# Kernel tuning notes

Measured on AMD Instinct MI355X. Metric: run time of the kernel, lower is better.

The kernel has to match this reference:

```python
import jax, jax.numpy as jnp
import numpy as np

N, E, H, ED, S = 20000, 320000, 256, 64, 4  # nodes, edges, hidden, edge_dim, message_steps


def setup_inputs() -> dict:
    key = jax.random.key(0)
    ks = jax.random.split(key, 20)
    w = lambda k, shape: jax.random.normal(k, shape, dtype=jnp.float32) * 0.02
    inp = {
        "node_state": jax.random.normal(ks[0], (N, H), dtype=jnp.float32),
        "edge_attr": jax.random.normal(ks[1], (E, ED), dtype=jnp.float32),
        # per-step stacked parameters (S steps)
        "nn_g": jnp.ones((S, H), jnp.float32),  # node_norm gamma
        "nn_b": jnp.zeros((S, H), jnp.float32),
        "mn_g": jnp.ones((S, H), jnp.float32),  # msg_norm gamma
        "mn_b": jnp.zeros((S, H), jnp.float32),
        "eW1": w(ks[2], (S, 2 * H + ED, H)), "eb1": jnp.zeros((S, H), jnp.float32),
        "eW2": w(ks[3], (S, H, H)),          "eb2": jnp.zeros((S, H), jnp.float32),
        "nW1": w(ks[4], (S, 2 * H, 2 * H)),  "nb1": jnp.zeros((S, 2 * H), jnp.float32),
        "nW2": w(ks[5], (S, 2 * H, H)),      "nb2": jnp.zeros((S, H), jnp.float32),
        "edge_index": jax.random.randint(ks[6], (2, E), 0, N, dtype=jnp.int64),
    }
    return inp


def _layer_norm(x, g, b, eps=1e-5):
    m = jnp.mean(x, axis=-1, keepdims=True)
    v = jnp.var(x, axis=-1, keepdims=True)
    return (x - m) * jax.lax.rsqrt(v + eps) * g + b


def reference(node_state, edge_attr, nn_g, nn_b, mn_g, mn_b,
              eW1, eb1, eW2, eb2, nW1, nb1, nW2, nb2, edge_index):
    n = node_state.shape[0]
    src, dst = edge_index[0], edge_index[1]
    ones = jnp.ones((dst.shape[0], 1), node_state.dtype)
    deg = jax.ops.segment_sum(ones, dst, num_segments=n)  # [N,1], same each step
    deg = jnp.maximum(deg, 1.0)
    h = node_state
    for i in range(nn_g.shape[0]):  # fixed small number of message steps
        hn = _layer_norm(h, nn_g[i], nn_b[i])                       # [N,H]
        x = jnp.concatenate([hn[src], hn[dst], edge_attr], axis=1)  # [E,2H+ED]
        msg = jax.nn.silu(x @ eW1[i] + eb1[i]) @ eW2[i] + eb2[i]    # [E,H]
        agg = jax.ops.segment_sum(msg, dst, num_segments=n)         # [N,H]
        agg = _layer_norm(agg / deg, mn_g[i], mn_b[i])
        y = jnp.concatenate([hn, agg], axis=1)                      # [N,2H]
        h = h + (jax.nn.silu(y @ nW1[i] + nb1[i]) @ nW2[i] + nb2[i])
    return h
```

## Files before the change

### kernel.cpp

```cpp
#include <hip/hip_runtime.h>
#include <hip/hip_bf16.h>
#include <stdint.h>

#define NN 20000
#define NE 320000
#define HH 256
#define EDK 64
#define NSTEPS 4
#define ECH 160000
#define NCHUNK 2
#define WSTEP 606208

typedef __attribute__((ext_vector_type(8))) short bf16x8;
typedef __attribute__((ext_vector_type(4))) float f32x4;

__device__ __forceinline__ float silu_f(float x) { return x / (1.0f + __expf(-x)); }

__device__ __forceinline__ unsigned short f2bf(float f) {
    __hip_bfloat16 h = __float2bfloat16(f);
    return __builtin_bit_cast(unsigned short, h);
}
__device__ __forceinline__ float bf2f(unsigned short u) {
    unsigned int x = ((unsigned int)u) << 16;
    return __builtin_bit_cast(float, x);
}
__device__ __forceinline__ unsigned int pk2(float a, float b) {
    return (unsigned int)f2bf(a) | ((unsigned int)f2bf(b) << 16);
}

__global__ void ln_kernel(const float* __restrict__ x, const float* __restrict__ g,
                          const float* __restrict__ b, unsigned short* __restrict__ y, int M)
{
    int row  = blockIdx.x * 4 + (threadIdx.x >> 6);
    int lane = threadIdx.x & 63;
    if (row >= M) return;
    float4 v = *(const float4*)(x + (size_t)row * HH + lane * 4);
    float s  = v.x + v.y + v.z + v.w;
    float ss = v.x*v.x + v.y*v.y + v.z*v.z + v.w*v.w;
#pragma unroll
    for (int off = 32; off > 0; off >>= 1) {
        s  += __shfl_down(s, off);
        ss += __shfl_down(ss, off);
    }
    float mean = __shfl(s, 0) * (1.0f / HH);
    float ms   = __shfl(ss, 0) * (1.0f / HH);
    float rstd = rsqrtf(ms - mean * mean + 1e-5f);
    float4 gg = *(const float4*)(g + lane * 4);
    float4 bb = *(const float4*)(b + lane * 4);
    ushort4 o;
    o.x = f2bf((v.x - mean) * rstd * gg.x + bb.x);
    o.y = f2bf((v.y - mean) * rstd * gg.y + bb.y);
    o.z = f2bf((v.z - mean) * rstd * gg.z + bb.z);
    o.w = f2bf((v.w - mean) * rstd * gg.w + bb.w);
    *(ushort4*)(y + (size_t)row * HH + lane * 4) = o;
}

__global__ void wtr_kernel(const float* __restrict__ eW1, const float* __restrict__ eW2,
                           const float* __restrict__ nW1, const float* __restrict__ nW2,
                           unsigned short* __restrict__ wbuf)
{
    int bx = blockIdx.x;
    int s  = bx / 592, t = bx % 592;
    const float* e1 = eW1 + (size_t)s * 576 * 256;
    unsigned short* wb = wbuf + (size_t)s * WSTEP;
    const float* src; unsigned short* dst; int K, N;
    if      (t < 64)  { src = e1;                          K = 256; N = 256; dst = wb; }
    else if (t < 128) { src = e1 + 65536;                  K = 256; N = 256; dst = wb + 65536;  t -= 64; }
    else if (t < 144) { src = e1 + 131072;                 K = 64;  N = 256; dst = wb + 131072; t -= 128; }
    else if (t < 208) { src = eW2 + (size_t)s * 65536;     K = 256; N = 256; dst = wb + 147456; t -= 144; }
    else if (t < 464) { src = nW1 + (size_t)s * 262144;    K = 512; N = 512; dst = wb + 212992; t -= 208; }
    else              { src = nW2 + (size_t)s * 131072;    K = 512; N = 256; dst = wb + 475136; t -= 464; }
    int ntn = N >> 5;
    int tk = t / ntn, tn = t % ntn;
    int k0 = tk * 32, n0 = tn * 32;
    __shared__ float ts[32][33];
    int tx = threadIdx.x & 31, ty = threadIdx.x >> 5;
#pragma unroll
    for (int i = 0; i < 4; i++)
        ts[ty + i * 8][tx] = src[(size_t)(k0 + ty + i * 8) * N + n0 + tx];
    __syncthreads();
#pragma unroll
    for (int i = 0; i < 4; i++)
        dst[(size_t)(n0 + ty + i * 8) * K + k0 + tx] = f2bf(ts[tx][ty + i * 8]);
}

__global__ void easort_kernel(const float* __restrict__ ea, const int* __restrict__ eorig,
                              unsigned short* __restrict__ out)
{
    int gid = blockIdx.x * 256 + threadIdx.x;
    int p = gid >> 4, q = gid & 15;
    if (p >= NE) return;
    float4 v = *(const float4*)(ea + (size_t)eorig[p] * EDK + q * 4);
    ushort4 o;
    o.x = f2bf(v.x); o.y = f2bf(v.y); o.z = f2bf(v.z); o.w = f2bf(v.w);
    *(ushort4*)(out + (size_t)p * EDK + q * 4) = o;
}

#define GBM 128
#define GBN 128
#define GBK 64
template <int EPI, int ASRC, bool BF16OUT>
__global__ __launch_bounds__(256) void mgemm(
    const void* __restrict__ A, const void* __restrict__ A2, int lda,
    const unsigned short* __restrict__ BT,
    const float* __restrict__ bias, const int* __restrict__ cnt,
    void* __restrict__ Cout, int M, int Nc, int K)
{
    __shared__ unsigned short smem[GBM * GBK + GBN * GBK];
    unsigned short* lsA = smem;
    unsigned short* lsB = smem + GBM * GBK;
    const int tid = threadIdx.x;
    const int row0 = blockIdx.x * GBM, col0 = blockIdx.y * GBN;
    const int r = tid >> 1, half = tid & 1;
    const int w = tid >> 6, l = tid & 63;
    const int wm = w >> 1, wn = w & 1;

    const float* Af = (const float*)A;
    const unsigned short* Ab = (const unsigned short*)A;
    const unsigned short* A2b = (const unsigned short*)A2;
    int grow = row0 + r;
    bool aval = (grow < M);
    const unsigned short* brow = BT + (size_t)(col0 + r) * K;

    f32x4 acc[4][4] = {};

    for (int k0 = 0; k0 < K; k0 += GBK) {
        if constexpr (ASRC == 3 || ASRC == 4) {
            uint4 q[4] = {};
            if (aval) {
                const unsigned short* ap;
                if constexpr (ASRC == 4)
                    ap = ((k0 < 256) ? Ab : A2b) + (size_t)grow * 256 + (k0 & 255) + half * 32;
                else
                    ap = Ab + (size_t)grow * lda + k0 + half * 32;
#pragma unroll
                for (int ci = 0; ci < 4; ci++) q[ci] = ((const uint4*)ap)[ci];
            }
#pragma unroll
            for (int ci = 0; ci < 4; ci++) {
                int slot = half * 4 + ci;
                int phys = slot ^ (r & 7);
                *(uint4*)&lsA[r * GBK + phys * 8] = q[ci];
            }
        } else {
            float4 fv[8];
            if (aval) {
                const float* ap = Af + (size_t)grow * lda + k0 + half * 32;
#pragma unroll
                for (int i = 0; i < 8; i++) fv[i] = ((const float4*)ap)[i];
            } else {
#pragma unroll
                for (int i = 0; i < 8; i++) fv[i] = make_float4(0.f, 0.f, 0.f, 0.f);
            }
#pragma unroll
            for (int ci = 0; ci < 4; ci++) {
                uint4 q;
                q.x = pk2(fv[2*ci].x,   fv[2*ci].y);
                q.y = pk2(fv[2*ci].z,   fv[2*ci].w);
                q.z = pk2(fv[2*ci+1].x, fv[2*ci+1].y);
                q.w = pk2(fv[2*ci+1].z, fv[2*ci+1].w);
                int slot = half * 4 + ci;
                int phys = slot ^ (r & 7);
                *(uint4*)&lsA[r * GBK + phys * 8] = q;
            }
        }
        {
            const unsigned short* bp = brow + k0 + half * 32;
#pragma unroll
            for (int ci = 0; ci < 4; ci++) {
                uint4 q = ((const uint4*)bp)[ci];
                int slot = half * 4 + ci;
                int phys = slot ^ (r & 7);
                *(uint4*)&lsB[r * GBK + phys * 8] = q;
            }
        }
        __syncthreads();
#pragma unroll
        for (int ks = 0; ks < 2; ks++) {
            bf16x8 bfr[4];
#pragma unroll
            for (int n = 0; n < 4; n++) {
                int rn = wn * 64 + n * 16 + (l & 15);
                int phys = (ks * 4 + (l >> 4)) ^ (rn & 7);
                bfr[n] = *(bf16x8*)&lsB[rn * GBK + phys * 8];
            }
#pragma unroll
            for (int m = 0; m < 4; m++) {
                int rm = wm * 64 + m * 16 + (l & 15);
                int phys = (ks * 4 + (l >> 4)) ^ (rm & 7);
                bf16x8 af = *(bf16x8*)&lsA[rm * GBK + phys * 8];
#pragma unroll
                for (int n = 0; n < 4; n++)
                    acc[m][n] = __builtin_amdgcn_mfma_f32_16x16x32_bf16(af, bfr[n], acc[m][n], 0, 0, 0);
            }
        }
        __syncthreads();
    }

    if constexpr (BF16OUT) {
        unsigned short* Cb = (unsigned short*)Cout;
#pragma unroll
        for (int n = 0; n < 4; n++) {
            int cl = wn * 64 + n * 16 + (l & 15);
            float bv = bias ? bias[col0 + cl] : 0.0f;
#pragma unroll
            for (int m = 0; m < 4; m++) {
                int rbase = wm * 64 + m * 16 + (l >> 4) * 4;
#pragma unroll
                for (int i = 0; i < 4; i++) {
                    int rl = rbase + i;
                    float o = acc[m][n][i] + bv;
                    if (EPI == 1) o = silu_f(o);
                    int chunk = cl >> 3;
                    int phys = chunk ^ (rl & 15);
                    smem[rl * 128 + phys * 8 + (cl & 7)] = f2bf(o);
                }
            }
        }
        __syncthreads();
        int orow = tid >> 1, hf = tid & 1;
        int rr = row0 + orow;
        if (rr < M) {
            unsigned short* crow = Cb + (size_t)rr * Nc + col0;
#pragma unroll
            for (int c8 = 0; c8 < 8; c8++) {
                int chunk = hf * 8 + c8;
                int phys = chunk ^ (orow & 15);
                uint4 v = *(uint4*)&smem[orow * 128 + phys * 8];
                *(uint4*)(crow + chunk * 8) = v;
            }
        }
    } else {
        float* Cf = (float*)Cout;
        const int cbase = col0 + wn * 64 + (l & 15);
#pragma unroll
        for (int n = 0; n < 4; n++) {
            int c = cbase + n * 16;
            float bv = bias ? bias[c] : 0.0f;
#pragma unroll
            for (int m = 0; m < 4; m++) {
                int rbase = row0 + wm * 64 + m * 16 + (l >> 4) * 4;
#pragma unroll
                for (int i = 0; i < 4; i++) {
                    int rr = rbase + i;
                    if (rr >= M) continue;
                    float o = acc[m][n][i];
                    if (EPI == 2) {
                        float cf = (float)cnt[rr];
                        o = (o + cf * bv) / fmaxf(cf, 1.0f);
                    } else {
                        o += bv;
                        if (EPI == 1) o = silu_f(o);
                    }
                    size_t off = (size_t)rr * Nc + c;
                    if (EPI == 3) Cf[off] += o;
                    else          Cf[off] = o;
                }
            }
        }
    }
}

template <bool FIRST>
__global__ void agg_kernel(const unsigned short* __restrict__ Pab,
                           const unsigned short* __restrict__ Pe, const int* __restrict__ esrc,
                           const int* __restrict__ rowptr,
                           unsigned short* __restrict__ u, int e0, int e1)
{
    int node = blockIdx.x * 4 + (threadIdx.x >> 6);
    if (node >= NN) return;
    int beg = rowptr[node], end = rowptr[node + 1];
    int lo = beg > e0 ? beg : e0;
    int hi = end < e1 ? end : e1;
    if (!FIRST && lo >= hi) return;
    int lane = threadIdx.x & 63;
    int j = lane * 4;
    float a0 = 0.f, a1 = 0.f, a2 = 0.f, a3 = 0.f;
    if (lo < hi) {
        ushort4 pb4 = *(const ushort4*)(Pab + (size_t)node * 512 + 256 + j);
        float b0 = bf2f(pb4.x), b1 = bf2f(pb4.y), b2 = bf2f(pb4.z), b3 = bf2f(pb4.w);
        int p = lo;
        int src = esrc[p];
        ushort4 pa = *(const ushort4*)(Pab + (size_t)src * 512 + j);
        ushort4 pe = *(const ushort4*)(Pe + (size_t)(p - e0) * HH + j);
        for (;;) {
            ushort4 cpa = pa, cpe = pe;
            int np = p + 1;
            if (np < hi) {
                int s2 = esrc[np];
                pa = *(const ushort4*)(Pab + (size_t)s2 * 512 + j);
                pe = *(const ushort4*)(Pe + (size_t)(np - e0) * HH + j);
            }
            a0 += silu_f(bf2f(cpa.x) + b0 + bf2f(cpe.x));
            a1 += silu_f(bf2f(cpa.y) + b1 + bf2f(cpe.y));
            a2 += silu_f(bf2f(cpa.z) + b2 + bf2f(cpe.z));
            a3 += silu_f(bf2f(cpa.w) + b3 + bf2f(cpe.w));
            if (np >= hi) break;
            p = np;
        }
    }
    unsigned short* up = u + (size_t)node * HH + j;
    if (!FIRST) {
        ushort4 uo = *(const ushort4*)up;
        a0 += bf2f(uo.x); a1 += bf2f(uo.y); a2 += bf2f(uo.z); a3 += bf2f(uo.w);
    }
    ushort4 o;
    o.x = f2bf(a0); o.y = f2bf(a1); o.z = f2bf(a2); o.w = f2bf(a3);
    *(ushort4*)up = o;
}

__global__ void detect_kernel(const uint32_t* __restrict__ w, int* flag)
{
    int i = blockIdx.x * 256 + threadIdx.x;
    bool bad = false;
    if (i < NE) {
        uint32_t lo = w[2 * i], hi = w[2 * i + 1];
        bad = (hi != 0u) || (lo >= (uint32_t)NN);
    }
    if (__any(bad)) {
        if ((threadIdx.x & 63) == 0) *flag = 0;
    }
}
__global__ void convert_kernel(const uint32_t* __restrict__ w, const int* __restrict__ flag,
                               int* __restrict__ out)
{
    int i = blockIdx.x * 256 + threadIdx.x;
    if (i >= 2 * NE) return;
    out[i] = (*flag) ? (int)w[2 * i] : (int)w[i];
}
__global__ void deg_kernel(const int* __restrict__ idx, int* __restrict__ cnt)
{
    int e = blockIdx.x * 256 + threadIdx.x;
    if (e < NE) atomicAdd(cnt + idx[NE + e], 1);
}

__global__ void scan_kernel(const int* __restrict__ cnt, int* __restrict__ rowptr)
{
    __shared__ int part[1024];
    const int T = 1024, PER = (NN + T - 1) / T;
    int t = threadIdx.x;
    int base = t * PER;
    int s = 0;
    for (int i = 0; i < PER; i++) {
        int idx = base + i;
        if (idx < NN) s += cnt[idx];
    }
    part[t] = s;
    __syncthreads();
    for (int off = 1; off < T; off <<= 1) {
        int v = (t >= off) ? part[t - off] : 0;
        __syncthreads();
        part[t] += v;
        __syncthreads();
    }
    int run = (t == 0) ? 0 : part[t - 1];
    for (int i = 0; i < PER; i++) {
        int idx = base + i;
        if (idx < NN) { rowptr[idx] = run; run += cnt[idx]; }
    }
    if (t == T - 1) rowptr[NN] = part[T - 1];
}

__global__ void fill_kernel(const int* __restrict__ idx, const int* __restrict__ rowptr,
                            int* __restrict__ fillc, int* __restrict__ esrc,
                            int* __restrict__ eorig)
{
    int e = blockIdx.x * 256 + threadIdx.x;
    if (e >= NE) return;
    int dst = idx[NE + e];
    int pos = rowptr[dst] + atomicAdd(fillc + dst, 1);
    esrc[pos]  = idx[e];
    eorig[pos] = e;
}

extern "C" void kernel_launch(void* const* d_in, const int* in_sizes, int n_in,
                              void* d_out, int out_size, void* d_ws, size_t ws_size,
                              hipStream_t stream)
{
    const float* node_state = (const float*)d_in[0];
    const float* edge_attr  = (const float*)d_in[1];
    const float* nn_g = (const float*)d_in[2];
    const float* nn_b = (const float*)d_in[3];
    const float* mn_g = (const float*)d_in[4];
    const float* mn_b = (const float*)d_in[5];
    const float* eW1  = (const float*)d_in[6];
    const float* eb1  = (const float*)d_in[7];
    const float* eW2  = (const float*)d_in[8];
    const float* eb2  = (const float*)d_in[9];
    const float* nW1  = (const float*)d_in[10];
    const float* nb1  = (const float*)d_in[11];
    const float* nW2  = (const float*)d_in[12];
    const float* nb2  = (const float*)d_in[13];
    const uint32_t* eidx_raw = (const uint32_t*)d_in[14];

    const size_t SZ = (size_t)NN * HH;
    unsigned short* hn  = (unsigned short*)d_ws;
    unsigned short* u   = hn + SZ;
    unsigned short* Pab = u + SZ;
    unsigned short* eas = Pab + (size_t)NN * 512;
    unsigned short* Pe  = eas + (size_t)NE * EDK;
    float* aggp = (float*)Pe;
    unsigned short* aggb = (unsigned short*)((char*)Pe + 22000000);
    unsigned short* zb   = (unsigned short*)((char*)Pe + 34000000);
    unsigned short* wbuf = Pe + (size_t)ECH * HH;
    int* idx32  = (int*)(wbuf + 4 * WSTEP);
    int* esrc   = idx32 + 2 * NE;
    int* eorig  = esrc + NE;
    int* rowptr = eorig + NE;
    int* cnt    = rowptr + NN + 1;
    int* fillc  = cnt + NN;
    int* flag   = fillc + NN;
    size_t needed = ((size_t)(flag + 1) - (size_t)d_ws);
    if (ws_size < needed) return;

    float* h = (float*)d_out;

    hipMemcpyAsync(h, node_state, SZ * sizeof(float), hipMemcpyDeviceToDevice, stream);

    wtr_kernel<<<4 * 592, 256, 0, stream>>>(eW1, eW2, nW1, nW2, wbuf);
    hipMemsetAsync(flag, 0xFF, sizeof(int), stream);
    detect_kernel<<<(NE + 255) / 256, 256, 0, stream>>>(eidx_raw, flag);
    convert_kernel<<<(2 * NE + 255) / 256, 256, 0, stream>>>(eidx_raw, flag, idx32);
    hipMemsetAsync(cnt, 0, NN * sizeof(int), stream);
    deg_kernel<<<(NE + 255) / 256, 256, 0, stream>>>(idx32, cnt);
    scan_kernel<<<1, 1024, 0, stream>>>(cnt, rowptr);
    hipMemsetAsync(fillc, 0, NN * sizeof(int), stream);
    fill_kernel<<<(NE + 255) / 256, 256, 0, stream>>>(idx32, rowptr, fillc, esrc, eorig);
    easort_kernel<<<(NE * 16) / 256, 256, 0, stream>>>(edge_attr, eorig, eas);

    const dim3 gN2((NN + GBM - 1) / GBM, 2);
    const dim3 gN4((NN + GBM - 1) / GBM, 4);
    const dim3 gPe(ECH / GBM, 2);

    for (int s = 0; s < NSTEPS; s++) {
        const unsigned short* wb = wbuf + (size_t)s * WSTEP;
        const unsigned short* WabT = wb;
        const unsigned short* WcT  = wb + 131072;
        const unsigned short* eW2T = wb + 147456;
        const unsigned short* nW1T = wb + 212992;
        const unsigned short* nW2T = wb + 475136;
        const float* eb1s = eb1 + (size_t)s * HH;
        const float* eb2s = eb2 + (size_t)s * HH;
        const float* nb1s = nb1 + (size_t)s * 512;
        const float* nb2s = nb2 + (size_t)s * HH;

        ln_kernel<<<NN / 4, 256, 0, stream>>>(h, nn_g + s * HH, nn_b + s * HH, hn, NN);
        mgemm<0, 3, true><<<gN4, 256, 0, stream>>>(hn, nullptr, HH, WabT, nullptr, nullptr, Pab, NN, 512, HH);
        {
            mgemm<0, 3, true><<<gPe, 256, 0, stream>>>(eas, nullptr, EDK, WcT, eb1s, nullptr, Pe, ECH, HH, EDK);
            agg_kernel<true><<<(NN + 3) / 4, 256, 0, stream>>>(Pab, Pe, esrc, rowptr, u, 0, ECH);
            mgemm<0, 3, true><<<gPe, 256, 0, stream>>>(eas + (size_t)ECH * EDK, nullptr, EDK, WcT, eb1s, nullptr, Pe, ECH, HH, EDK);
            agg_kernel<false><<<(NN + 3) / 4, 256, 0, stream>>>(Pab, Pe, esrc, rowptr, u, ECH, NE);
        }
        mgemm<2, 3, false><<<gN2, 256, 0, stream>>>(u, nullptr, HH, eW2T, eb2s, cnt, aggp, NN, HH, HH);
        ln_kernel<<<NN / 4, 256, 0, stream>>>(aggp, mn_g + s * HH, mn_b + s * HH, aggb, NN);
        mgemm<1, 4, true><<<gN4, 256, 0, stream>>>(hn, aggb, HH, nW1T, nb1s, nullptr, zb, NN, 512, 512);
        mgemm<3, 3, false><<<gN2, 256, 0, stream>>>(zb, nullptr, 512, nW2T, nb2s, nullptr, h, NN, HH, 512);
    }
}
```

Before: 1.690 ms.

## Register-prefetch next GEMM tile and let edge GEMM blocks process two M-tiles

Restructures the bf16 GEMM main loop so the global loads for the next K-slice (or next M-tile) go into registers while the MFMAs for the current slice run, overlapping memory latency with compute. Adds a TM template parameter so one block walks several M-tiles with a fused epilogue per tile. The edge-attribute GEMM now uses two tiles per block with half as many blocks. The unused fp32 A-source path is removed. The prefetch raises register pressure and may lower occupancy, and the smaller edge grid gives less parallelism.

```diff
diff --git a/kernel.cpp b/kernel.cpp
--- a/kernel.cpp
+++ b/kernel.cpp
@@ -8,7 +8,6 @@
 #define EDK 64
 #define NSTEPS 4
 #define ECH 160000
-#define NCHUNK 2
 #define WSTEP 606208
 
 typedef __attribute__((ext_vector_type(8))) short bf16x8;
@@ -23,9 +22,6 @@
 __device__ __forceinline__ float bf2f(unsigned short u) {
     unsigned int x = ((unsigned int)u) << 16;
     return __builtin_bit_cast(float, x);
-}
-__device__ __forceinline__ unsigned int pk2(float a, float b) {
-    return (unsigned int)f2bf(a) | ((unsigned int)f2bf(b) << 16);
 }
 
 __global__ void ln_kernel(const float* __restrict__ x, const float* __restrict__ g,
@@ -99,7 +95,7 @@
 #define GBM 128
 #define GBN 128
 #define GBK 64
-template <int EPI, int ASRC, bool BF16OUT>
+template <int EPI, int ASRC, bool BF16OUT, int TM>
 __global__ __launch_bounds__(256) void mgemm(
     const void* __restrict__ A, const void* __restrict__ A2, int lda,
     const unsigned short* __restrict__ BT,
@@ -110,71 +106,56 @@
     unsigned short* lsA = smem;
     unsigned short* lsB = smem + GBM * GBK;
     const int tid = threadIdx.x;
-    const int row0 = blockIdx.x * GBM, col0 = blockIdx.y * GBN;
+    const int col0 = blockIdx.y * GBN;
     const int r = tid >> 1, half = tid & 1;
     const int w = tid >> 6, l = tid & 63;
     const int wm = w >> 1, wn = w & 1;
-
-    const float* Af = (const float*)A;
-    const unsigned short* Ab = (const unsigned short*)A;
+    const int bx0 = blockIdx.x * TM;
+
+    const unsigned short* Ab  = (const unsigned short*)A;
     const unsigned short* A2b = (const unsigned short*)A2;
-    int grow = row0 + r;
-    bool aval = (grow < M);
     const unsigned short* brow = BT + (size_t)(col0 + r) * K;
 
+    const int KI = K >> 6;
+    const int NIT = TM * KI;
+
+    uint4 cA[4], cB[4], nA[4], nB[4];
+
+    auto loadAB = [&](int mt2, int k0, uint4* dA, uint4* dB) {
+        int grow = (bx0 + mt2) * GBM + r;
+        if (grow < M) {
+            const unsigned short* ap;
+            if constexpr (ASRC == 4)
+                ap = ((k0 < 256) ? Ab : A2b) + (size_t)grow * 256 + (k0 & 255) + half * 32;
+            else
+                ap = Ab + (size_t)grow * lda + k0 + half * 32;
+#pragma unroll
+            for (int ci = 0; ci < 4; ci++) dA[ci] = ((const uint4*)ap)[ci];
+        } else {
+#pragma unroll
+            for (int ci = 0; ci < 4; ci++) dA[ci] = make_uint4(0, 0, 0, 0);
+        }
+        const unsigned short* bp = brow + k0 + half * 32;
+#pragma unroll
+        for (int ci = 0; ci < 4; ci++) dB[ci] = ((const uint4*)bp)[ci];
+    };
+
     f32x4 acc[4][4] = {};
-
-    for (int k0 = 0; k0 < K; k0 += GBK) {
-        if constexpr (ASRC == 3 || ASRC == 4) {
-            uint4 q[4] = {};
-            if (aval) {
-                const unsigned short* ap;
-                if constexpr (ASRC == 4)
-                    ap = ((k0 < 256) ? Ab : A2b) + (size_t)grow * 256 + (k0 & 255) + half * 32;
-                else
-                    ap = Ab + (size_t)grow * lda + k0 + half * 32;
-#pragma unroll
-                for (int ci = 0; ci < 4; ci++) q[ci] = ((const uint4*)ap)[ci];
-            }
-#pragma unroll
-            for (int ci = 0; ci < 4; ci++) {
-                int slot = half * 4 + ci;
-                int phys = slot ^ (r & 7);
-                *(uint4*)&lsA[r * GBK + phys * 8] = q[ci];
-            }
-        } else {
-            float4 fv[8];
-            if (aval) {
-                const float* ap = Af + (size_t)grow * lda + k0 + half * 32;
-#pragma unroll
-                for (int i = 0; i < 8; i++) fv[i] = ((const float4*)ap)[i];
-            } else {
-#pragma unroll
-                for (int i = 0; i < 8; i++) fv[i] = make_float4(0.f, 0.f, 0.f, 0.f);
-            }
-#pragma unroll
-            for (int ci = 0; ci < 4; ci++) {
-                uint4 q;
-                q.x = pk2(fv[2*ci].x,   fv[2*ci].y);
-                q.y = pk2(fv[2*ci].z,   fv[2*ci].w);
-                q.z = pk2(fv[2*ci+1].x, fv[2*ci+1].y);
-                q.w = pk2(fv[2*ci+1].z, fv[2*ci+1].w);
-                int slot = half * 4 + ci;
-                int phys = slot ^ (r & 7);
-                *(uint4*)&lsA[r * GBK + phys * 8] = q;
-            }
-        }
-        {
-            const unsigned short* bp = brow + k0 + half * 32;
-#pragma unroll
-            for (int ci = 0; ci < 4; ci++) {
-                uint4 q = ((const uint4*)bp)[ci];
-                int slot = half * 4 + ci;
-                int phys = slot ^ (r & 7);
-                *(uint4*)&lsB[r * GBK + phys * 8] = q;
-            }
+    loadAB(0, 0, cA, cB);
+
+    int mt = 0, ki = 0;
+    for (int it = 0; it < NIT; ++it) {
+#pragma unroll
+        for (int ci = 0; ci < 4; ci++) {
+            int slot = half * 4 + ci;
+            int phys = slot ^ (r & 7);
+            *(uint4*)&lsA[r * GBK + phys * 8] = cA[ci];
+            *(uint4*)&lsB[r * GBK + phys * 8] = cB[ci];
         }
         __syncthreads();
+        int nki = ki + 1, nmt = mt;
+        if (nki == KI) { nki = 0; ++nmt; }
+        if (nmt < TM) loadAB(nmt, nki << 6, nA, nB);
 #pragma unroll
         for (int ks = 0; ks < 2; ks++) {
             bf16x8 bfr[4];
@@ -195,69 +176,82 @@
             }
         }
         __syncthreads();
-    }
-
-    if constexpr (BF16OUT) {
-        unsigned short* Cb = (unsigned short*)Cout;
-#pragma unroll
-        for (int n = 0; n < 4; n++) {
-            int cl = wn * 64 + n * 16 + (l & 15);
-            float bv = bias ? bias[col0 + cl] : 0.0f;
-#pragma unroll
-            for (int m = 0; m < 4; m++) {
-                int rbase = wm * 64 + m * 16 + (l >> 4) * 4;
-#pragma unroll
-                for (int i = 0; i < 4; i++) {
-                    int rl = rbase + i;
-                    float o = acc[m][n][i] + bv;
-                    if (EPI == 1) o = silu_f(o);
-                    int chunk = cl >> 3;
-                    int phys = chunk ^ (rl & 15);
-                    smem[rl * 128 + phys * 8 + (cl & 7)] = f2bf(o);
+
+        if (ki == KI - 1) {
+            const int row0 = (bx0 + mt) * GBM;
+            if constexpr (BF16OUT) {
+                unsigned short* Cb = (unsigned short*)Cout;
+#pragma unroll
+                for (int n = 0; n < 4; n++) {
+                    int cl = wn * 64 + n * 16 + (l & 15);
+                    float bv = bias ? bias[col0 + cl] : 0.0f;
+#pragma unroll
+                    for (int m = 0; m < 4; m++) {
+                        int rbase = wm * 64 + m * 16 + (l >> 4) * 4;
+#pragma unroll
+                        for (int i = 0; i < 4; i++) {
+                            int rl = rbase + i;
+                            float o = acc[m][n][i] + bv;
+                            if (EPI == 1) o = silu_f(o);
+                            int chunk = cl >> 3;
+                            int phys = chunk ^ (rl & 15);
+                            smem[rl * 128 + phys * 8 + (cl & 7)] = f2bf(o);
+                        }
+                    }
+                }
+                __syncthreads();
+                int orow = tid >> 1, hf = tid & 1;
+                int rr = row0 + orow;
+                if (rr < M) {
+                    unsigned short* crow = Cb + (size_t)rr * Nc + col0;
+#pragma unroll
+                    for (int c8 = 0; c8 < 8; c8++) {
+                        int chunk = hf * 8 + c8;
+                        int phys = chunk ^ (orow & 15);
+                        uint4 v = *(uint4*)&smem[orow * 128 + phys * 8];
+                        *(uint4*)(crow + chunk * 8) = v;
+                    }
+                }
+                __syncthreads();
+            } else {
+                float* Cf = (float*)Cout;
+                const int cbase = col0 + wn * 64 + (l & 15);
+#pragma unroll
+                for (int n = 0; n < 4; n++) {
+                    int c = cbase + n * 16;
+                    float bv = bias ? bias[c] : 0.0f;
+#pragma unroll
+                    for (int m = 0; m < 4; m++) {
+                        int rbase = row0 + wm * 64 + m * 16 + (l >> 4) * 4;
+#pragma unroll
+                        for (int i = 0; i < 4; i++) {
+                            int rr = rbase + i;
+                            if (rr >= M) continue;
+                            float o = acc[m][n][i];
+                            if (EPI == 2) {
+                                float cf = (float)cnt[rr];
+                                o = (o + cf * bv) / fmaxf(cf, 1.0f);
+                            } else {
+                                o += bv;
+                                if (EPI == 1) o = silu_f(o);
+                            }
+                            size_t off = (size_t)rr * Nc + c;
+                            if (EPI == 3) Cf[off] += o;
+                            else          Cf[off] = o;
+                        }
+                    }
                 }
             }
-        }
-        __syncthreads();
-        int orow = tid >> 1, hf = tid & 1;
-        int rr = row0 + orow;
-        if (rr < M) {
-            unsigned short* crow = Cb + (size_t)rr * Nc + col0;
-#pragma unroll
-            for (int c8 = 0; c8 < 8; c8++) {
-                int chunk = hf * 8 + c8;
-                int phys = chunk ^ (orow & 15);
-                uint4 v = *(uint4*)&smem[orow * 128 + phys * 8];
-                *(uint4*)(crow + chunk * 8) = v;
+            if (it + 1 < NIT) {
+#pragma unroll
+                for (int m = 0; m < 4; m++)
+#pragma unroll
+                    for (int n = 0; n < 4; n++) acc[m][n] = f32x4{0.f, 0.f, 0.f, 0.f};
             }
         }
-    } else {
-        float* Cf = (float*)Cout;
-        const int cbase = col0 + wn * 64 + (l & 15);
-#pragma unroll
-        for (int n = 0; n < 4; n++) {
-            int c = cbase + n * 16;
-            float bv = bias ? bias[c] : 0.0f;
-#pragma unroll
-            for (int m = 0; m < 4; m++) {
-                int rbase = row0 + wm * 64 + m * 16 + (l >> 4) * 4;
-#pragma unroll
-                for (int i = 0; i < 4; i++) {
-                    int rr = rbase + i;
-                    if (rr >= M) continue;
-                    float o = acc[m][n][i];
-                    if (EPI == 2) {
-                        float cf = (float)cnt[rr];
-                        o = (o + cf * bv) / fmaxf(cf, 1.0f);
-                    } else {
-                        o += bv;
-                        if (EPI == 1) o = silu_f(o);
-                    }
-                    size_t off = (size_t)rr * Nc + c;
-                    if (EPI == 3) Cf[off] += o;
-                    else          Cf[off] = o;
-                }
-            }
-        }
+        if (++ki == KI) { ki = 0; ++mt; }
+#pragma unroll
+        for (int ci = 0; ci < 4; ci++) { cA[ci] = nA[ci]; cB[ci] = nB[ci]; }
     }
 }
 
@@ -430,7 +424,7 @@
 
     const dim3 gN2((NN + GBM - 1) / GBM, 2);
     const dim3 gN4((NN + GBM - 1) / GBM, 4);
-    const dim3 gPe(ECH / GBM, 2);
+    const dim3 gPe(ECH / (GBM * 2), 2);
 
     for (int s = 0; s < NSTEPS; s++) {
         const unsigned short* wb = wbuf + (size_t)s * WSTEP;
@@ -445,16 +439,16 @@
         const float* nb2s = nb2 + (size_t)s * HH;
 
         ln_kernel<<<NN / 4, 256, 0, stream>>>(h, nn_g + s * HH, nn_b + s * HH, hn, NN);
-        mgemm<0, 3, true><<<gN4, 256, 0, stream>>>(hn, nullptr, HH, WabT, nullptr, nullptr, Pab, NN, 512, HH);
+        mgemm<0, 3, true, 1><<<gN4, 256, 0, stream>>>(hn, nullptr, HH, WabT, nullptr, nullptr, Pab, NN, 512, HH);
         {
-            mgemm<0, 3, true><<<gPe, 256, 0, stream>>>(eas, nullptr, EDK, WcT, eb1s, nullptr, Pe, ECH, HH, EDK);
+            mgemm<0, 3, true, 2><<<gPe, 256, 0, stream>>>(eas, nullptr, EDK, WcT, eb1s, nullptr, Pe, ECH, HH, EDK);
             agg_kernel<true><<<(NN + 3) / 4, 256, 0, stream>>>(Pab, Pe, esrc, rowptr, u, 0, ECH);
-            mgemm<0, 3, true><<<gPe, 256, 0, stream>>>(eas + (size_t)ECH * EDK, nullptr, EDK, WcT, eb1s, nullptr, Pe, ECH, HH, EDK);
+            mgemm<0, 3, true, 2><<<gPe, 256, 0, stream>>>(eas + (size_t)ECH * EDK, nullptr, EDK, WcT, eb1s, nullptr, Pe, ECH, HH, EDK);
             agg_kernel<false><<<(NN + 3) / 4, 256, 0, stream>>>(Pab, Pe, esrc, rowptr, u, ECH, NE);
         }
-        mgemm<2, 3, false><<<gN2, 256, 0, stream>>>(u, nullptr, HH, eW2T, eb2s, cnt, aggp, NN, HH, HH);
+        mgemm<2, 3, false, 1><<<gN2, 256, 0, stream>>>(u, nullptr, HH, eW2T, eb2s, cnt, aggp, NN, HH, HH);
         ln_kernel<<<NN / 4, 256, 0, stream>>>(aggp, mn_g + s * HH, mn_b + s * HH, aggb, NN);
-        mgemm<1, 4, true><<<gN4, 256, 0, stream>>>(hn, aggb, HH, nW1T, nb1s, nullptr, zb, NN, 512, 512);
-        mgemm<3, 3, false><<<gN2, 256, 0, stream>>>(zb, nullptr, 512, nW2T, nb2s, nullptr, h, NN, HH, 512);
-    }
-}
+        mgemm<1, 4, true, 1><<<gN4, 256, 0, stream>>>(hn, aggb, HH, nW1T, nb1s, nullptr, zb, NN, 512, 512);
+        mgemm<3, 3, false, 1><<<gN2, 256, 0, stream>>>(zb, nullptr, 512, nW2T, nb2s, nullptr, h, NN, HH, 512);
+    }
+}
```

Result: slower. 2.042 ms (+20.9%).

## Fuse node and edge projection GEMMs into one launch; use narrower N tiles

Applied to the files above, without the earlier changes.

Merges the node projection GEMM (hn x WabT) and the first edge-attribute chunk GEMM into a single dual_kernel launch, with block IDs split between the two problems. This removes one launch and lets the small node GEMM share the GPU with the larger edge GEMM. The N-dimension GEMMs (eW2, nW1, nW2) move to 64-column tiles, doubling grid size for better CU occupancy on the 20000-row problems, at the cost of more A-tile reloads. The unused fp32-A path is removed.

```diff
diff --git a/kernel.cpp b/kernel.cpp
--- a/kernel.cpp
+++ b/kernel.cpp
@@ -8,8 +8,8 @@
 #define EDK 64
 #define NSTEPS 4
 #define ECH 160000
-#define NCHUNK 2
 #define WSTEP 606208
+#define MT1 157
 
 typedef __attribute__((ext_vector_type(8))) short bf16x8;
 typedef __attribute__((ext_vector_type(4))) float f32x4;
@@ -23,9 +23,6 @@
 __device__ __forceinline__ float bf2f(unsigned short u) {
     unsigned int x = ((unsigned int)u) << 16;
     return __builtin_bit_cast(float, x);
-}
-__device__ __forceinline__ unsigned int pk2(float a, float b) {
-    return (unsigned int)f2bf(a) | ((unsigned int)f2bf(b) << 16);
 }
 
 __global__ void ln_kernel(const float* __restrict__ x, const float* __restrict__ g,
@@ -97,90 +94,72 @@
 }
 
 #define GBM 128
-#define GBN 128
 #define GBK 64
-template <int EPI, int ASRC, bool BF16OUT>
-__global__ __launch_bounds__(256) void mgemm(
+template <int EPI, int ASRC, bool BF16OUT, int GBNT>
+__device__ __forceinline__ void mgemm_body(
+    int bxv, int byv,
     const void* __restrict__ A, const void* __restrict__ A2, int lda,
     const unsigned short* __restrict__ BT,
     const float* __restrict__ bias, const int* __restrict__ cnt,
     void* __restrict__ Cout, int M, int Nc, int K)
 {
-    __shared__ unsigned short smem[GBM * GBK + GBN * GBK];
+    constexpr int NF   = GBNT / 32;
+    constexpr int TPRB = 8 / NF;
+    constexpr int CPR  = GBNT / 8;
+    __shared__ unsigned short smem[(GBM + GBNT) * GBK];
     unsigned short* lsA = smem;
     unsigned short* lsB = smem + GBM * GBK;
     const int tid = threadIdx.x;
-    const int row0 = blockIdx.x * GBM, col0 = blockIdx.y * GBN;
-    const int r = tid >> 1, half = tid & 1;
+    const int col0 = byv * GBNT;
+    const int rA = tid >> 1, half = tid & 1;
+    const int rB = tid / TPRB, subB = tid % TPRB;
     const int w = tid >> 6, l = tid & 63;
     const int wm = w >> 1, wn = w & 1;
 
-    const float* Af = (const float*)A;
-    const unsigned short* Ab = (const unsigned short*)A;
+    const unsigned short* Ab  = (const unsigned short*)A;
     const unsigned short* A2b = (const unsigned short*)A2;
-    int grow = row0 + r;
-    bool aval = (grow < M);
-    const unsigned short* brow = BT + (size_t)(col0 + r) * K;
-
-    f32x4 acc[4][4] = {};
+    const int growA = bxv * GBM + rA;
+    const bool aval = (growA < M);
+    const unsigned short* brow = BT + (size_t)(col0 + rB) * K;
+
+    f32x4 acc[4][NF] = {};
 
     for (int k0 = 0; k0 < K; k0 += GBK) {
-        if constexpr (ASRC == 3 || ASRC == 4) {
+        {
             uint4 q[4] = {};
             if (aval) {
                 const unsigned short* ap;
                 if constexpr (ASRC == 4)
-                    ap = ((k0 < 256) ? Ab : A2b) + (size_t)grow * 256 + (k0 & 255) + half * 32;
+                    ap = ((k0 < 256) ? Ab : A2b) + (size_t)growA * 256 + (k0 & 255) + half * 32;
                 else
-                    ap = Ab + (size_t)grow * lda + k0 + half * 32;
+                    ap = Ab + (size_t)growA * lda + k0 + half * 32;
 #pragma unroll
                 for (int ci = 0; ci < 4; ci++) q[ci] = ((const uint4*)ap)[ci];
             }
 #pragma unroll
             for (int ci = 0; ci < 4; ci++) {
                 int slot = half * 4 + ci;
-                int phys = slot ^ (r & 7);
-                *(uint4*)&lsA[r * GBK + phys * 8] = q[ci];
-            }
-        } else {
-            float4 fv[8];
-            if (aval) {
-                const float* ap = Af + (size_t)grow * lda + k0 + half * 32;
-#pragma unroll
-                for (int i = 0; i < 8; i++) fv[i] = ((const float4*)ap)[i];
-            } else {
-#pragma unroll
-                for (int i = 0; i < 8; i++) fv[i] = make_float4(0.f, 0.f, 0.f, 0.f);
-            }
-#pragma unroll
-            for (int ci = 0; ci < 4; ci++) {
-                uint4 q;
-                q.x = pk2(fv[2*ci].x,   fv[2*ci].y);
-                q.y = pk2(fv[2*ci].z,   fv[2*ci].w);
-                q.z = pk2(fv[2*ci+1].x, fv[2*ci+1].y);
-                q.w = pk2(fv[2*ci+1].z, fv[2*ci+1].w);
-                int slot = half * 4 + ci;
-                int phys = slot ^ (r & 7);
-                *(uint4*)&lsA[r * GBK + phys * 8] = q;
+                int phys = slot ^ (rA & 7);
+                *(uint4*)&lsA[rA * GBK + phys * 8] = q[ci];
             }
         }
         {
-            const unsigned short* bp = brow + k0 + half * 32;
-#pragma unroll
-            for (int ci = 0; ci < 4; ci++) {
+            const unsigned short* bp = brow + k0 + subB * (NF * 8);
+#pragma unroll
+            for (int ci = 0; ci < NF; ci++) {
                 uint4 q = ((const uint4*)bp)[ci];
-                int slot = half * 4 + ci;
-                int phys = slot ^ (r & 7);
-                *(uint4*)&lsB[r * GBK + phys * 8] = q;
+                int slot = subB * NF + ci;
+                int phys = slot ^ (rB & 7);
+                *(uint4*)&lsB[rB * GBK + phys * 8] = q;
             }
         }
         __syncthreads();
 #pragma unroll
         for (int ks = 0; ks < 2; ks++) {
-            bf16x8 bfr[4];
-#pragma unroll
-            for (int n = 0; n < 4; n++) {
-                int rn = wn * 64 + n * 16 + (l & 15);
+            bf16x8 bfr[NF];
+#pragma unroll
+            for (int n = 0; n < NF; n++) {
+                int rn = wn * (GBNT / 2) + n * 16 + (l & 15);
                 int phys = (ks * 4 + (l >> 4)) ^ (rn & 7);
                 bfr[n] = *(bf16x8*)&lsB[rn * GBK + phys * 8];
             }
@@ -190,18 +169,19 @@
                 int phys = (ks * 4 + (l >> 4)) ^ (rm & 7);
                 bf16x8 af = *(bf16x8*)&lsA[rm * GBK + phys * 8];
 #pragma unroll
-                for (int n = 0; n < 4; n++)
+                for (int n = 0; n < NF; n++)
                     acc[m][n] = __builtin_amdgcn_mfma_f32_16x16x32_bf16(af, bfr[n], acc[m][n], 0, 0, 0);
             }
         }
         __syncthreads();
     }
 
+    const int row0 = bxv * GBM;
     if constexpr (BF16OUT) {
         unsigned short* Cb = (unsigned short*)Cout;
 #pragma unroll
-        for (int n = 0; n < 4; n++) {
-            int cl = wn * 64 + n * 16 + (l & 15);
+        for (int n = 0; n < NF; n++) {
+            int cl = wn * (GBNT / 2) + n * 16 + (l & 15);
             float bv = bias ? bias[col0 + cl] : 0.0f;
 #pragma unroll
             for (int m = 0; m < 4; m++) {
@@ -212,8 +192,8 @@
                     float o = acc[m][n][i] + bv;
                     if (EPI == 1) o = silu_f(o);
                     int chunk = cl >> 3;
-                    int phys = chunk ^ (rl & 15);
-                    smem[rl * 128 + phys * 8 + (cl & 7)] = f2bf(o);
+                    int phys = chunk ^ (rl & (CPR - 1));
+                    smem[rl * GBNT + phys * 8 + (cl & 7)] = f2bf(o);
                 }
             }
         }
@@ -223,18 +203,18 @@
         if (rr < M) {
             unsigned short* crow = Cb + (size_t)rr * Nc + col0;
 #pragma unroll
-            for (int c8 = 0; c8 < 8; c8++) {
-                int chunk = hf * 8 + c8;
-                int phys = chunk ^ (orow & 15);
-                uint4 v = *(uint4*)&smem[orow * 128 + phys * 8];
+            for (int c8 = 0; c8 < CPR / 2; c8++) {
+                int chunk = hf * (CPR / 2) + c8;
+                int phys = chunk ^ (orow & (CPR - 1));
+                uint4 v = *(uint4*)&smem[orow * GBNT + phys * 8];
                 *(uint4*)(crow + chunk * 8) = v;
             }
         }
     } else {
         float* Cf = (float*)Cout;
-        const int cbase = col0 + wn * 64 + (l & 15);
-#pragma unroll
-        for (int n = 0; n < 4; n++) {
+        const int cbase = col0 + wn * (GBNT / 2) + (l & 15);
+#pragma unroll
+        for (int n = 0; n < NF; n++) {
             int c = cbase + n * 16;
             float bv = bias ? bias[c] : 0.0f;
 #pragma unroll
@@ -259,6 +239,38 @@
             }
         }
     }
+}
+
+template <int EPI, int ASRC, bool BF16OUT, int GBNT>
+__global__ __launch_bounds__(256) void mgemm(
+    const void* __restrict__ A, const void* __restrict__ A2, int lda,
+    const unsigned short* __restrict__ BT,
+    const float* __restrict__ bias, const int* __restrict__ cnt,
+    void* __restrict__ Cout, int M, int Nc, int K)
+{
+    mgemm_body<EPI, ASRC, BF16OUT, GBNT>(blockIdx.x, blockIdx.y, A, A2, lda, BT, bias, cnt,
+                                         Cout, M, Nc, K);
+}
+
+__global__ __launch_bounds__(256) void dual_kernel(
+    const unsigned short* __restrict__ hn, const unsigned short* __restrict__ WabT,
+    unsigned short* __restrict__ Pab,
+    const unsigned short* __restrict__ eas, const unsigned short* __restrict__ WcT,
+    const float* __restrict__ eb1s, unsigned short* __restrict__ Pe)
+{
+    const int split = MT1 * 4;
+    int bid = blockIdx.x;
+    int bx, by, lda, M, Nc, K;
+    const void* A; const unsigned short* BT; const float* bias; void* C;
+    if (bid < split) {
+        bx = bid % MT1; by = bid / MT1;
+        A = hn; lda = HH; BT = WabT; bias = nullptr; C = Pab; M = NN; Nc = 512; K = HH;
+    } else {
+        int id2 = bid - split;
+        bx = id2 % (ECH / GBM); by = id2 / (ECH / GBM);
+        A = eas; lda = EDK; BT = WcT; bias = eb1s; C = Pe; M = ECH; Nc = HH; K = EDK;
+    }
+    mgemm_body<0, 3, true, 128>(bx, by, A, nullptr, lda, BT, bias, nullptr, C, M, Nc, K);
 }
 
 template <bool FIRST>
@@ -428,8 +440,7 @@
     fill_kernel<<<(NE + 255) / 256, 256, 0, stream>>>(idx32, rowptr, fillc, esrc, eorig);
     easort_kernel<<<(NE * 16) / 256, 256, 0, stream>>>(edge_attr, eorig, eas);
 
-    const dim3 gN2((NN + GBM - 1) / GBM, 2);
-    const dim3 gN4((NN + GBM - 1) / GBM, 4);
+    const int nDual = MT1 * 4 + (ECH / GBM) * 2;
     const dim3 gPe(ECH / GBM, 2);
 
     for (int s = 0; s < NSTEPS; s++) {
@@ -445,16 +456,13 @@
         const float* nb2s = nb2 + (size_t)s * HH;
 
         ln_kernel<<<NN / 4, 256, 0, stream>>>(h, nn_g + s * HH, nn_b + s * HH, hn, NN);
-        mgemm<0, 3, true><<<gN4, 256, 0, stream>>>(hn, nullptr, HH, WabT, nullptr, nullptr, Pab, NN, 512, HH);
-        {
-            mgemm<0, 3, true><<<gPe, 256, 0, stream>>>(eas, nullptr, EDK, WcT, eb1s, nullptr, Pe, ECH, HH, EDK);
-            agg_kernel<true><<<(NN + 3) / 4, 256, 0, stream>>>(Pab, Pe, esrc, rowptr, u, 0, ECH);
-            mgemm<0, 3, true><<<gPe, 256, 0, stream>>>(eas + (size_t)ECH * EDK, nullptr, EDK, WcT, eb1s, nullptr, Pe, ECH, HH, EDK);
-            agg_kernel<false><<<(NN + 3) / 4, 256, 0, stream>>>(Pab, Pe, esrc, rowptr, u, ECH, NE);
-        }
-        mgemm<2, 3, false><<<gN2, 256, 0, stream>>>(u, nullptr, HH, eW2T, eb2s, cnt, aggp, NN, HH, HH);
+        dual_kernel<<<nDual, 256, 0, stream>>>(hn, WabT, Pab, eas, WcT, eb1s, Pe);
+        agg_kernel<true><<<(NN + 3) / 4, 256, 0, stream>>>(Pab, Pe, esrc, rowptr, u, 0, ECH);
+        mgemm<0, 3, true, 128><<<gPe, 256, 0, stream>>>(eas + (size_t)ECH * EDK, nullptr, EDK, WcT, eb1s, nullptr, Pe, ECH, HH, EDK);
+        agg_kernel<false><<<(NN + 3) / 4, 256, 0, stream>>>(Pab, Pe, esrc, rowptr, u, ECH, NE);
+        mgemm<2, 3, false, 64><<<dim3(MT1, 4), 256, 0, stream>>>(u, nullptr, HH, eW2T, eb2s, cnt, aggp, NN, HH, HH);
         ln_kernel<<<NN / 4, 256, 0, stream>>>(aggp, mn_g + s * HH, mn_b + s * HH, aggb, NN);
-        mgemm<1, 4, true><<<gN4, 256, 0, stream>>>(hn, aggb, HH, nW1T, nb1s, nullptr, zb, NN, 512, 512);
-        mgemm<3, 3, false><<<gN2, 256, 0, stream>>>(zb, nullptr, 512, nW2T, nb2s, nullptr, h, NN, HH, 512);
-    }
-}
+        mgemm<1, 4, true, 64><<<dim3(MT1, 8), 256, 0, stream>>>(hn, aggb, HH, nW1T, nb1s, nullptr, zb, NN, 512, 512);
+        mgemm<3, 3, false, 64><<<dim3(MT1, 4), 256, 0, stream>>>(zb, nullptr, 512, nW2T, nb2s, nullptr, h, NN, HH, 512);
+    }
+}
```

Measured after the change: 1.721 ms. About the same (+1.9%).
